# Optimization experiments

Measured on AMD Instinct MI355X. Metric: run time of the kernel, lower is better.

## Reference

```python
import jax, jax.numpy as jnp
import numpy as np

N_NODES = 50000
N_EDGES = 1_600_000
C = 128
K = 10


def setup_inputs() -> dict:
    key = jax.random.key(0)
    k1, k2, k3, k4 = jax.random.split(key, 4)
    x = jax.random.normal(k1, (N_NODES, C), dtype=jnp.float32)
    coeffs = jax.random.normal(k2, (K + 1,), dtype=jnp.float32) * 0.3
    src = jax.random.randint(k3, (N_EDGES,), 0, N_NODES, dtype=jnp.int64)
    dst = jax.random.randint(k4, (N_EDGES,), 0, N_NODES, dtype=jnp.int64)
    edge_index = jnp.stack([src, dst], axis=0)
    return {"x": x, "coeffs": coeffs, "edge_index": edge_index}


def _gcn_norm(edge_index, num_nodes, dtype):
    """Add self-loops, return (src, dst, norm) with norm = d^-1/2[src]*d^-1/2[dst]."""
    loop = jnp.arange(num_nodes, dtype=edge_index.dtype)
    src = jnp.concatenate([edge_index[0], loop])
    dst = jnp.concatenate([edge_index[1], loop])
    ones = jnp.ones(src.shape[0], dtype=dtype)
    deg = jax.ops.segment_sum(ones, dst, num_segments=num_nodes)
    dinv = jnp.where(deg > 0, jax.lax.rsqrt(deg), 0.0).astype(dtype)
    norm = dinv[src] * dinv[dst]  # [E+N]
    return src, dst, norm


def reference(x, coeffs, edge_index):
    """GPR/Arnoldi polynomial propagation:
       hidden = sum_{k=0..K} coeffs[k] * A_hat^k x, A_hat = D^-1/2 (A+I) D^-1/2."""
    n = x.shape[0]
    src, dst, norm = _gcn_norm(edge_index, n, x.dtype)

    def step(carry, gamma):
        xc, hid = carry
        msg = xc[src] * norm[:, None]                       # gather + scale
        xn = jax.ops.segment_sum(msg, dst, num_segments=n)  # scatter-add
        return (xn, hid + gamma * xn), None

    hidden0 = coeffs[0] * x
    (_, hidden), _ = jax.lax.scan(step, (x, hidden0), coeffs[1:])
    return hidden
```

## Files before the change

### kernel.cpp

```cpp
#include <hip/hip_runtime.h>
#include <hip/hip_fp16.h>

#define C 128
#define HC 64
#define NBUCK 256
#define NSLICE 8
#define NCHUNK 512
#define BCH 64
#define MAXNPS 8192

typedef float f4_t __attribute__((ext_vector_type(4)));

__global__ __launch_bounds__(256)
void pcount_kernel(const int* __restrict__ dst, int* __restrict__ pcnt, int E, int nps) {
    int chunk = blockIdx.x;
    const int per = (E + NCHUNK - 1) / NCHUNK;
    int beg = chunk * per;
    int end = beg + per; if (end > E) end = E;
    __shared__ int lc[NSLICE];
    if (threadIdx.x < NSLICE) lc[threadIdx.x] = 0;
    __syncthreads();
    for (int e = beg + threadIdx.x; e < end; e += 256) {
        int s = dst[e] / nps;
        atomicAdd(&lc[s], 1);
    }
    __syncthreads();
    if (threadIdx.x < NSLICE) pcnt[chunk * NSLICE + threadIdx.x] = lc[threadIdx.x];
}

__global__ __launch_bounds__(256)
void pscan_kernel(const int* __restrict__ pcnt, int* __restrict__ poffs,
                  int* __restrict__ sbase, int E) {
    __shared__ int part[256];
    int t = threadIdx.x;
    int vals[16];
    int sum = 0;
    #pragma unroll
    for (int i = 0; i < 16; ++i) {
        int key = t * 16 + i;
        int s = key >> 9;
        int c = key & (NCHUNK - 1);
        vals[i] = pcnt[c * NSLICE + s];
        sum += vals[i];
    }
    part[t] = sum;
    __syncthreads();
    for (int off = 1; off < 256; off <<= 1) {
        int v = 0;
        if (t >= off) v = part[t - off];
        __syncthreads();
        if (t >= off) part[t] += v;
        __syncthreads();
    }
    int run = (t == 0) ? 0 : part[t - 1];
    #pragma unroll
    for (int i = 0; i < 16; ++i) {
        poffs[t * 16 + i] = run;
        run += vals[i];
    }
    __syncthreads();
    if (t < NSLICE) sbase[t] = poffs[t << 9];
    if (t == NSLICE) sbase[NSLICE] = E;
}

__global__ __launch_bounds__(256)
void ppart_kernel(const int* __restrict__ src, const int* __restrict__ dst,
                  const int* __restrict__ poffs, unsigned int* __restrict__ pedges,
                  int E, int nps) {
    int chunk = blockIdx.x;
    const int per = (E + NCHUNK - 1) / NCHUNK;
    int beg = chunk * per;
    int end = beg + per; if (end > E) end = E;
    __shared__ int lcur[NSLICE];
    if (threadIdx.x < NSLICE) lcur[threadIdx.x] = poffs[threadIdx.x * NCHUNK + chunk];
    __syncthreads();
    for (int e = beg + threadIdx.x; e < end; e += 256) {
        int d = dst[e];
        int s = d / nps;
        int pos = atomicAdd(&lcur[s], 1);
        pedges[pos] = ((unsigned)(d - s * nps) << 16) | (unsigned)src[e];
    }
}

__global__ __launch_bounds__(256)
void bcount_kernel(const unsigned int* __restrict__ pedges, const int* __restrict__ sbase,
                   int* __restrict__ phist, int N, int nps) {
    int s = blockIdx.x & 7;
    int c = blockIdx.x >> 3;
    int lo = sbase[s], hi = sbase[s + 1];
    int len = hi - lo;
    int per = (len + BCH - 1) / BCH;
    int beg = lo + c * per;
    int end = beg + per; if (end > hi) end = hi;
    __shared__ int h[MAXNPS];
    int base_node = s * nps;
    int nn = nps; if (base_node + nn > N) nn = N - base_node;
    for (int i = threadIdx.x; i < nn; i += 256) h[i] = 0;
    __syncthreads();
    for (int e = beg + threadIdx.x; e < end; e += 256) {
        unsigned int u = pedges[e];
        atomicAdd(&h[u >> 16], 1);
    }
    __syncthreads();
    int* out = phist + (size_t)c * N + base_node;
    for (int i = threadIdx.x; i < nn; i += 256) out[i] = h[i];
}

__global__ void merge1_kernel(const int* __restrict__ phist, int* __restrict__ cnt, int N) {
    int i = blockIdx.x * blockDim.x + threadIdx.x;
    if (i >= N) return;
    int s = 0;
    #pragma unroll 8
    for (int c = 0; c < BCH; ++c) s += phist[(size_t)c * N + i];
    cnt[i] = s;
}

__global__ void merge2_kernel(const int* __restrict__ phist, const int* __restrict__ offsets,
                              int* __restrict__ pbase, int N) {
    int i = blockIdx.x * blockDim.x + threadIdx.x;
    if (i >= N) return;
    int run = offsets[i];
    #pragma unroll 8
    for (int c = 0; c < BCH; ++c) {
        pbase[(size_t)c * N + i] = run;
        run += phist[(size_t)c * N + i];
    }
}

__global__ __launch_bounds__(256)
void pscatter_kernel(const unsigned int* __restrict__ pedges, const int* __restrict__ sbase,
                     const int* __restrict__ pbase, unsigned short* __restrict__ srcs16,
                     int N, int nps) {
    int s = blockIdx.x & 7;
    int c = blockIdx.x >> 3;
    int lo = sbase[s], hi = sbase[s + 1];
    int len = hi - lo;
    int per = (len + BCH - 1) / BCH;
    int beg = lo + c * per;
    int end = beg + per; if (end > hi) end = hi;
    __shared__ int lcur[MAXNPS];
    int base_node = s * nps;
    int nn = nps; if (base_node + nn > N) nn = N - base_node;
    const int* pb = pbase + (size_t)c * N + base_node;
    for (int i = threadIdx.x; i < nn; i += 256) lcur[i] = pb[i];
    __syncthreads();
    for (int e = beg + threadIdx.x; e < end; e += 256) {
        unsigned int u = pedges[e];
        int pos = atomicAdd(&lcur[u >> 16], 1);
        srcs16[pos] = (unsigned short)(u & 0xffffu);
    }
}

__global__ void scan_reduce_kernel(const int* __restrict__ cnt, int* __restrict__ psum, int n) {
    __shared__ int s[256];
    int t = threadIdx.x;
    int i = blockIdx.x * 256 + t;
    s[t] = (i < n) ? cnt[i] : 0;
    __syncthreads();
    for (int off = 128; off > 0; off >>= 1) {
        if (t < off) s[t] += s[t + off];
        __syncthreads();
    }
    if (t == 0) psum[blockIdx.x] = s[0];
}

__global__ void scan_partials_kernel(const int* __restrict__ psum, int* __restrict__ bpre,
                                     int* __restrict__ offsets, int n, int nb) {
    __shared__ int s[256];
    int t = threadIdx.x;
    s[t] = (t < nb) ? psum[t] : 0;
    __syncthreads();
    for (int off = 1; off < 256; off <<= 1) {
        int v = 0;
        if (t >= off) v = s[t - off];
        __syncthreads();
        if (t >= off) s[t] += v;
        __syncthreads();
    }
    bpre[t] = (t == 0) ? 0 : s[t - 1];
    if (t == 255) offsets[n] = s[255];
}

__global__ void scan_apply_kernel(const int* __restrict__ cnt, const int* __restrict__ bpre,
                                  int* __restrict__ offsets, int* __restrict__ cursor,
                                  float* __restrict__ dinv, int n) {
    __shared__ int s[256];
    int t = threadIdx.x;
    int i = blockIdx.x * 256 + t;
    int c = (i < n) ? cnt[i] : 0;
    s[t] = c;
    __syncthreads();
    for (int off = 1; off < 256; off <<= 1) {
        int v = 0;
        if (t >= off) v = s[t - off];
        __syncthreads();
        if (t >= off) s[t] += v;
        __syncthreads();
    }
    if (i < n) {
        int excl = bpre[blockIdx.x] + s[t] - c;
        offsets[i] = excl;
        cursor[i]  = excl;
        dinv[i]    = rsqrtf((float)(c + 1));
    }
}

__global__ void hist_zero_kernel(int* __restrict__ hist) { hist[threadIdx.x] = 0; }

__global__ void hist_kernel(const int* __restrict__ cnt, int* __restrict__ hist, int n) {
    __shared__ int lh[NBUCK];
    int t = threadIdx.x;
    lh[t] = 0;
    __syncthreads();
    for (int i = blockIdx.x * blockDim.x + t; i < n; i += gridDim.x * blockDim.x) {
        int d = cnt[i]; if (d > NBUCK - 1) d = NBUCK - 1;
        atomicAdd(&lh[d], 1);
    }
    __syncthreads();
    int c = lh[t];
    if (c) atomicAdd(&hist[t], c);
}

__global__ void hist_scan_kernel(const int* __restrict__ hist, int* __restrict__ bcur) {
    __shared__ int s[256];
    int t = threadIdx.x;
    s[t] = hist[t];
    __syncthreads();
    for (int off = 1; off < 256; off <<= 1) {
        int v = 0;
        if (t >= off) v = s[t - off];
        __syncthreads();
        if (t >= off) s[t] += v;
        __syncthreads();
    }
    bcur[t] = (t == 0) ? 0 : s[t - 1];
}

__global__ void perm_kernel(const int* __restrict__ cnt, int* __restrict__ bcur,
                            int* __restrict__ perm, int n) {
    __shared__ int lhist[NBUCK];
    __shared__ int lbase[NBUCK];
    int t = threadIdx.x;
    lhist[t] = 0;
    __syncthreads();
    int i = blockIdx.x * 256 + t;
    int d = 0, lr = 0;
    if (i < n) {
        d = cnt[i]; if (d > NBUCK - 1) d = NBUCK - 1;
        lr = atomicAdd(&lhist[d], 1);
    }
    __syncthreads();
    int c = lhist[t];
    if (c > 0) lbase[t] = atomicAdd(&bcur[t], c);
    __syncthreads();
    if (i < n) perm[lbase[d] + lr] = i;
}

__global__ void zero_cnt_kernel(int* __restrict__ cnt, int n) {
    int i = blockIdx.x * blockDim.x + threadIdx.x;
    if (i < n) cnt[i] = 0;
}

__global__ void count_kernel(const int* __restrict__ dst, int* __restrict__ cnt,
                             int E, int nps) {
    int slice = blockIdx.x & 7;
    int chunk = blockIdx.x >> 3;
    int nchunks = gridDim.x >> 3;
    int per = (E + nchunks - 1) / nchunks;
    int beg = chunk * per;
    int end = beg + per; if (end > E) end = E;
    int lo = slice * nps, hi = lo + nps;
    for (int e = beg + threadIdx.x; e < end; e += blockDim.x) {
        int d = dst[e];
        if (d >= lo && d < hi) atomicAdd(&cnt[d], 1);
    }
}

__global__ void scatter_kernel(const int* __restrict__ src, const int* __restrict__ dst,
                               int* __restrict__ cursor, int* __restrict__ sorted_src,
                               int E, int nps) {
    int slice = blockIdx.x & 7;
    int chunk = blockIdx.x >> 3;
    int nchunks = gridDim.x >> 3;
    int per = (E + nchunks - 1) / nchunks;
    int beg = chunk * per;
    int end = beg + per; if (end > E) end = E;
    int lo = slice * nps, hi = lo + nps;
    for (int e = beg + threadIdx.x; e < end; e += blockDim.x) {
        int d = dst[e];
        if (d >= lo && d < hi) {
            int pos = atomicAdd(&cursor[d], 1);
            sorted_src[pos] = src[e];
        }
    }
}

__global__ void init_kernel(const float* __restrict__ x, const float* __restrict__ coeffs,
                            const float* __restrict__ dinv, float* __restrict__ hidden,
                            unsigned short* __restrict__ ya, unsigned short* __restrict__ yb,
                            int N) {
    int i = blockIdx.x * blockDim.x + threadIdx.x;
    if (i >= N * 16) return;
    int node = i >> 4;
    int g = i & 15;
    float dv = dinv[node];
    const float4* xp = (const float4*)(x + (size_t)node * C + g * 8);
    float4 x0 = xp[0], x1 = xp[1];
    if (hidden) {
        float g0 = coeffs[0];
        float4* hp = (float4*)(hidden + (size_t)node * C + g * 8);
        hp[0] = make_float4(g0 * x0.x, g0 * x0.y, g0 * x0.z, g0 * x0.w);
        hp[1] = make_float4(g0 * x1.x, g0 * x1.y, g0 * x1.z, g0 * x1.w);
    }
    __half2 p0 = __floats2half2_rn(dv * x0.x, dv * x0.y);
    __half2 p1 = __floats2half2_rn(dv * x0.z, dv * x0.w);
    __half2 p2 = __floats2half2_rn(dv * x1.x, dv * x1.y);
    __half2 p3 = __floats2half2_rn(dv * x1.z, dv * x1.w);
    uint4 u;
    u.x = *reinterpret_cast<unsigned int*>(&p0);
    u.y = *reinterpret_cast<unsigned int*>(&p1);
    u.z = *reinterpret_cast<unsigned int*>(&p2);
    u.w = *reinterpret_cast<unsigned int*>(&p3);
    unsigned short* yp = (g < 8) ? ya : yb;
    int jj = g & 7;
    ((uint4*)yp)[(size_t)node * 8 + jj] = u;
}

__device__ __forceinline__ void acc8(float* a, uint4 u) {
    __half2* h = (__half2*)&u;
    #pragma unroll
    for (int i = 0; i < 4; ++i) {
        float2 f = __half22float2(h[i]);
        a[2 * i]     += f.x;
        a[2 * i + 1] += f.y;
    }
}

template<typename IdxT>
__global__ __launch_bounds__(256)
void prop2_kernel(const unsigned short* __restrict__ yin0, const unsigned short* __restrict__ yin1,
                  unsigned short* __restrict__ yout0, unsigned short* __restrict__ yout1,
                  float* __restrict__ hidden, const float* __restrict__ coeffs, int k,
                  const int* __restrict__ offsets, const IdxT* __restrict__ srcs,
                  const float* __restrict__ dinv, const int* __restrict__ perm, int n) {
    int bid  = blockIdx.x;
    int xcd  = bid & 7;
    int half = xcd >> 2;
    int q    = (bid >> 3) * 4 + (xcd & 3);
    int t = threadIdx.x;
    int lane = t & 63;
    int grp  = lane >> 3;
    int j    = lane & 7;
    int slot = q * 32 + (t >> 6) * 8 + grp;
    if (slot >= n) return;
    int v = perm[slot];
    int beg = offsets[v];
    int end = offsets[v + 1];
    float dv = dinv[v];
    float gamma = coeffs[k];

    const uint4* base = (const uint4*)(half ? yin1 : yin0);
    float A0[8] = {0,0,0,0,0,0,0,0};
    float A1[8] = {0,0,0,0,0,0,0,0};
    float A2[8] = {0,0,0,0,0,0,0,0};
    float A3[8] = {0,0,0,0,0,0,0,0};

    int e = beg;
    for (; e + 8 <= end; e += 8) {
        int s0 = (int)srcs[e],     s1 = (int)srcs[e + 1];
        int s2 = (int)srcs[e + 2], s3 = (int)srcs[e + 3];
        int s4 = (int)srcs[e + 4], s5 = (int)srcs[e + 5];
        int s6 = (int)srcs[e + 6], s7 = (int)srcs[e + 7];
        uint4 u0 = base[(size_t)s0 * 8 + j];
        uint4 u1 = base[(size_t)s1 * 8 + j];
        uint4 u2 = base[(size_t)s2 * 8 + j];
        uint4 u3 = base[(size_t)s3 * 8 + j];
        uint4 u4 = base[(size_t)s4 * 8 + j];
        uint4 u5 = base[(size_t)s5 * 8 + j];
        uint4 u6 = base[(size_t)s6 * 8 + j];
        uint4 u7 = base[(size_t)s7 * 8 + j];
        acc8(A0, u0); acc8(A1, u1); acc8(A2, u2); acc8(A3, u3);
        acc8(A0, u4); acc8(A1, u5); acc8(A2, u6); acc8(A3, u7);
    }
    for (; e + 4 <= end; e += 4) {
        int s0 = (int)srcs[e],     s1 = (int)srcs[e + 1];
        int s2 = (int)srcs[e + 2], s3 = (int)srcs[e + 3];
        uint4 u0 = base[(size_t)s0 * 8 + j];
        uint4 u1 = base[(size_t)s1 * 8 + j];
        uint4 u2 = base[(size_t)s2 * 8 + j];
        uint4 u3 = base[(size_t)s3 * 8 + j];
        acc8(A0, u0); acc8(A1, u1); acc8(A2, u2); acc8(A3, u3);
    }
    for (; e < end; ++e) {
        uint4 u = base[(size_t)srcs[e] * 8 + j];
        acc8(A0, u);
    }
    uint4 us = base[(size_t)v * 8 + j];
    acc8(A1, us);

    float xn[8];
    #pragma unroll
    for (int i = 0; i < 8; ++i)
        xn[i] = dv * ((A0[i] + A1[i]) + (A2[i] + A3[i]));

    if (hidden) {
        f4_t* hp = (f4_t*)(hidden + (size_t)v * C + half * HC + j * 8);
        f4_t h0 = __builtin_nontemporal_load(hp);
        f4_t h1 = __builtin_nontemporal_load(hp + 1);
        h0.x += gamma * xn[0]; h0.y += gamma * xn[1]; h0.z += gamma * xn[2]; h0.w += gamma * xn[3];
        h1.x += gamma * xn[4]; h1.y += gamma * xn[5]; h1.z += gamma * xn[6]; h1.w += gamma * xn[7];
        __builtin_nontemporal_store(h0, hp);
        __builtin_nontemporal_store(h1, hp + 1);
    }

    __half2 p0 = __floats2half2_rn(dv * xn[0], dv * xn[1]);
    __half2 p1 = __floats2half2_rn(dv * xn[2], dv * xn[3]);
    __half2 p2 = __floats2half2_rn(dv * xn[4], dv * xn[5]);
    __half2 p3 = __floats2half2_rn(dv * xn[6], dv * xn[7]);
    uint4 u;
    u.x = *reinterpret_cast<unsigned int*>(&p0);
    u.y = *reinterpret_cast<unsigned int*>(&p1);
    u.z = *reinterpret_cast<unsigned int*>(&p2);
    u.w = *reinterpret_cast<unsigned int*>(&p3);
    unsigned short* yout = half ? yout1 : yout0;
    ((uint4*)yout)[(size_t)v * 8 + j] = u;
}

__global__ void final_kernel(const float* __restrict__ x, const float* __restrict__ coeffs,
                             const float* __restrict__ dinv, const unsigned short* __restrict__ ybig,
                             float* __restrict__ hidden, int N, int K) {
    int i = blockIdx.x * blockDim.x + threadIdx.x;
    if (i >= N * 16) return;
    int node = i >> 4;
    int g = i & 15;
    int half = g >> 3;
    int jj = g & 7;
    float g0 = coeffs[0];
    float rdv = 1.0f / dinv[node];
    const float4* xp = (const float4*)(x + (size_t)node * C + g * 8);
    float4 x0 = xp[0], x1 = xp[1];
    float a[8] = {g0 * x0.x, g0 * x0.y, g0 * x0.z, g0 * x0.w,
                  g0 * x1.x, g0 * x1.y, g0 * x1.z, g0 * x1.w};
    const uint4* yb = (const uint4*)ybig;
    size_t bstride = (size_t)N * 8;
    size_t row = (size_t)node * 8 + jj;
    for (int k = 1; k <= K; ++k) {
        float s = coeffs[k] * rdv;
        uint4 u = yb[(size_t)(2 * k + half) * bstride + row];
        __half2* h = (__half2*)&u;
        #pragma unroll
        for (int q2 = 0; q2 < 4; ++q2) {
            float2 f = __half22float2(h[q2]);
            a[2 * q2]     += s * f.x;
            a[2 * q2 + 1] += s * f.y;
        }
    }
    float4* hp = (float4*)(hidden + (size_t)node * C + g * 8);
    hp[0] = make_float4(a[0], a[1], a[2], a[3]);
    hp[1] = make_float4(a[4], a[5], a[6], a[7]);
}

extern "C" void kernel_launch(void* const* d_in, const int* in_sizes, int n_in,
                              void* d_out, int out_size, void* d_ws, size_t ws_size,
                              hipStream_t stream) {
    const float* x      = (const float*)d_in[0];
    const float* coeffs = (const float*)d_in[1];
    const int*   edge   = (const int*)d_in[2];

    const int N = in_sizes[0] / C;
    const int K = in_sizes[1] - 1;
    const int E = in_sizes[2] / 2;
    const int* src = edge;
    const int* dst = edge + E;

    char* ws = (char*)d_ws;
    auto alloc = [&](size_t bytes) -> void* {
        void* p = (void*)ws;
        ws += (bytes + 255) & ~(size_t)255;
        return p;
    };
    int*   cnt        = (int*)alloc((size_t)N * 4);
    int*   offsets    = (int*)alloc((size_t)(N + 1) * 4);
    int*   cursor     = (int*)alloc((size_t)N * 4);
    int*   sorted_src = (int*)alloc((size_t)E * 4);
    float* dinv       = (float*)alloc((size_t)N * 4);
    int*   psum       = (int*)alloc(256 * 4);
    int*   bpre       = (int*)alloc(256 * 4);
    int*   hist       = (int*)alloc(NBUCK * 4);
    int*   bcur       = (int*)alloc(NBUCK * 4);
    int*   perm       = (int*)alloc((size_t)N * 4);
    unsigned short* srcs16 = (unsigned short*)alloc((size_t)E * 2);
    unsigned int*   pedges = (unsigned int*)alloc((size_t)E * 4);
    int*   pcnt   = (int*)alloc((size_t)NCHUNK * NSLICE * 4);
    int*   poffs  = (int*)alloc((size_t)NCHUNK * NSLICE * 4);
    int*   sbase  = (int*)alloc((NSLICE + 1) * 4);
    int*   phist  = (int*)alloc((size_t)BCH * N * 4);
    int*   pbase  = (int*)alloc((size_t)BCH * N * 4);

    const size_t NBelems  = (size_t)N * HC;
    const size_t bufbytes = NBelems * 2;
    size_t misc_used = (size_t)(ws - (char*)d_ws);
    const int nbuf_deferred = 2 * (K + 1);
    bool deferred = (ws_size >= misc_used + (size_t)nbuf_deferred * bufbytes + 4096);
    unsigned short* ybig = (unsigned short*)alloc((size_t)(deferred ? nbuf_deferred : 4) * bufbytes);
    auto ybuf = [&](int p, int h) -> unsigned short* {
        return ybig + ((size_t)(2 * p + h)) * NBelems;
    };

    const int B = 256;
    const int nb = (N + 255) / 256;
    const int nps = (N + NSLICE - 1) / NSLICE;
    const bool fastpre = (N <= 65536) && (nps <= MAXNPS);

    if (fastpre) {
        pcount_kernel<<<NCHUNK, B, 0, stream>>>(dst, pcnt, E, nps);
        pscan_kernel<<<1, B, 0, stream>>>(pcnt, poffs, sbase, E);
        ppart_kernel<<<NCHUNK, B, 0, stream>>>(src, dst, poffs, pedges, E, nps);
        bcount_kernel<<<8 * BCH, B, 0, stream>>>(pedges, sbase, phist, N, nps);
        merge1_kernel<<<nb, B, 0, stream>>>(phist, cnt, N);
        scan_reduce_kernel<<<nb, 256, 0, stream>>>(cnt, psum, N);
        scan_partials_kernel<<<1, 256, 0, stream>>>(psum, bpre, offsets, N, nb);
        scan_apply_kernel<<<nb, 256, 0, stream>>>(cnt, bpre, offsets, cursor, dinv, N);
        merge2_kernel<<<nb, B, 0, stream>>>(phist, offsets, pbase, N);
        hist_zero_kernel<<<1, NBUCK, 0, stream>>>(hist);
        hist_kernel<<<64, 256, 0, stream>>>(cnt, hist, N);
        hist_scan_kernel<<<1, NBUCK, 0, stream>>>(hist, bcur);
        perm_kernel<<<nb, 256, 0, stream>>>(cnt, bcur, perm, N);
        pscatter_kernel<<<8 * BCH, B, 0, stream>>>(pedges, sbase, pbase, srcs16, N, nps);
    } else {
        const int slice_grid = 8 * 256;
        zero_cnt_kernel<<<(N + B - 1) / B, B, 0, stream>>>(cnt, N);
        count_kernel<<<slice_grid, B, 0, stream>>>(dst, cnt, E, nps);
        scan_reduce_kernel<<<nb, 256, 0, stream>>>(cnt, psum, N);
        scan_partials_kernel<<<1, 256, 0, stream>>>(psum, bpre, offsets, N, nb);
        scan_apply_kernel<<<nb, 256, 0, stream>>>(cnt, bpre, offsets, cursor, dinv, N);
        hist_zero_kernel<<<1, NBUCK, 0, stream>>>(hist);
        hist_kernel<<<64, 256, 0, stream>>>(cnt, hist, N);
        hist_scan_kernel<<<1, NBUCK, 0, stream>>>(hist, bcur);
        perm_kernel<<<nb, 256, 0, stream>>>(cnt, bcur, perm, N);
        scatter_kernel<<<slice_grid, B, 0, stream>>>(src, dst, cursor, sorted_src, E, nps);
    }

    float* hidden = (float*)d_out;
    float* hid_for_prop = deferred ? nullptr : hidden;
    init_kernel<<<((size_t)N * 16 + B - 1) / B, B, 0, stream>>>(
        x, coeffs, dinv, hid_for_prop, ybuf(0, 0), ybuf(0, 1), N);

    const int pgrid = (N + 31) / 32;
    const int grid2 = 8 * ((pgrid + 3) / 4);
    for (int k = 1; k <= K; ++k) {
        int pin  = deferred ? (k - 1) : ((k - 1) & 1);
        int pout = deferred ? k       : (k & 1);
        if (fastpre) {
            prop2_kernel<unsigned short><<<grid2, B, 0, stream>>>(
                ybuf(pin, 0), ybuf(pin, 1), ybuf(pout, 0), ybuf(pout, 1),
                hid_for_prop, coeffs, k, offsets, srcs16, dinv, perm, N);
        } else {
            prop2_kernel<int><<<grid2, B, 0, stream>>>(
                ybuf(pin, 0), ybuf(pin, 1), ybuf(pout, 0), ybuf(pout, 1),
                hid_for_prop, coeffs, k, offsets, sorted_src, dinv, perm, N);
        }
    }

    if (deferred) {
        final_kernel<<<((size_t)N * 16 + B - 1) / B, B, 0, stream>>>(
            x, coeffs, dinv, ybig, hidden, N, K);
    }
}
```

Before: 588.2 us.

## Pre-partition edges by source slice before destination partitioning; reverse degree-bucket order

Adds a first partition pass that groups edges by source-node slice into a packed dst<<16|src buffer. The existing destination partition then runs over this buffer, so within each destination slice the sources come out roughly ordered by slice. The aim is better gather locality on the x rows during propagation. It also changes the degree-bucket scan to give descending offsets, so high-degree nodes are scheduled first. This costs three extra preprocessing launches and one more E-sized buffer pass.

New measurement: 541.6 us. 7.9% less time.

```diff
diff --git a/kernel.cpp b/kernel.cpp
--- a/kernel.cpp
+++ b/kernel.cpp
@@ -11,8 +11,9 @@
 
 typedef float f4_t __attribute__((ext_vector_type(4)));
 
-__global__ __launch_bounds__(256)
-void pcount_kernel(const int* __restrict__ dst, int* __restrict__ pcnt, int E, int nps) {
+
+__global__ __launch_bounds__(256)
+void s0count_kernel(const int* __restrict__ src, int* __restrict__ s0cnt, int E, int snps) {
     int chunk = blockIdx.x;
     const int per = (E + NCHUNK - 1) / NCHUNK;
     int beg = chunk * per;
@@ -21,11 +22,30 @@
     if (threadIdx.x < NSLICE) lc[threadIdx.x] = 0;
     __syncthreads();
     for (int e = beg + threadIdx.x; e < end; e += 256) {
-        int s = dst[e] / nps;
+        int s = src[e] / snps;
         atomicAdd(&lc[s], 1);
     }
     __syncthreads();
-    if (threadIdx.x < NSLICE) pcnt[chunk * NSLICE + threadIdx.x] = lc[threadIdx.x];
+    if (threadIdx.x < NSLICE) s0cnt[chunk * NSLICE + threadIdx.x] = lc[threadIdx.x];
+}
+
+__global__ __launch_bounds__(256)
+void s0part_kernel(const int* __restrict__ src, const int* __restrict__ dst,
+                   const int* __restrict__ s0offs, unsigned int* __restrict__ edges0,
+                   int E, int snps) {
+    int chunk = blockIdx.x;
+    const int per = (E + NCHUNK - 1) / NCHUNK;
+    int beg = chunk * per;
+    int end = beg + per; if (end > E) end = E;
+    __shared__ int lcur[NSLICE];
+    if (threadIdx.x < NSLICE) lcur[threadIdx.x] = s0offs[threadIdx.x * NCHUNK + chunk];
+    __syncthreads();
+    for (int e = beg + threadIdx.x; e < end; e += 256) {
+        int sv = src[e];
+        int s = sv / snps;
+        int pos = atomicAdd(&lcur[s], 1);
+        edges0[pos] = ((unsigned)dst[e] << 16) | (unsigned)sv;
+    }
 }
 
 __global__ __launch_bounds__(256)
@@ -64,9 +84,26 @@
 }
 
 __global__ __launch_bounds__(256)
-void ppart_kernel(const int* __restrict__ src, const int* __restrict__ dst,
-                  const int* __restrict__ poffs, unsigned int* __restrict__ pedges,
-                  int E, int nps) {
+void pcount2_kernel(const unsigned int* __restrict__ edges0, int* __restrict__ pcnt,
+                    int E, int nps) {
+    int chunk = blockIdx.x;
+    const int per = (E + NCHUNK - 1) / NCHUNK;
+    int beg = chunk * per;
+    int end = beg + per; if (end > E) end = E;
+    __shared__ int lc[NSLICE];
+    if (threadIdx.x < NSLICE) lc[threadIdx.x] = 0;
+    __syncthreads();
+    for (int e = beg + threadIdx.x; e < end; e += 256) {
+        int s = (int)(edges0[e] >> 16) / nps;
+        atomicAdd(&lc[s], 1);
+    }
+    __syncthreads();
+    if (threadIdx.x < NSLICE) pcnt[chunk * NSLICE + threadIdx.x] = lc[threadIdx.x];
+}
+
+__global__ __launch_bounds__(256)
+void ppart2_kernel(const unsigned int* __restrict__ edges0, const int* __restrict__ poffs,
+                   unsigned int* __restrict__ pedges, int E, int nps) {
     int chunk = blockIdx.x;
     const int per = (E + NCHUNK - 1) / NCHUNK;
     int beg = chunk * per;
@@ -75,10 +112,11 @@
     if (threadIdx.x < NSLICE) lcur[threadIdx.x] = poffs[threadIdx.x * NCHUNK + chunk];
     __syncthreads();
     for (int e = beg + threadIdx.x; e < end; e += 256) {
-        int d = dst[e];
+        unsigned int u = edges0[e];
+        int d = (int)(u >> 16);
         int s = d / nps;
         int pos = atomicAdd(&lcur[s], 1);
-        pedges[pos] = ((unsigned)(d - s * nps) << 16) | (unsigned)src[e];
+        pedges[pos] = ((unsigned)(d - s * nps) << 16) | (u & 0xffffu);
     }
 }
 
@@ -233,7 +271,8 @@
         if (t >= off) s[t] += v;
         __syncthreads();
     }
-    bcur[t] = (t == 0) ? 0 : s[t - 1];
+    int total = s[255];
+    bcur[t] = total - s[t];
 }
 
 __global__ void perm_kernel(const int* __restrict__ cnt, int* __restrict__ bcur,
@@ -491,9 +530,13 @@
     int*   perm       = (int*)alloc((size_t)N * 4);
     unsigned short* srcs16 = (unsigned short*)alloc((size_t)E * 2);
     unsigned int*   pedges = (unsigned int*)alloc((size_t)E * 4);
+    unsigned int*   edges0 = (unsigned int*)alloc((size_t)E * 4);
     int*   pcnt   = (int*)alloc((size_t)NCHUNK * NSLICE * 4);
     int*   poffs  = (int*)alloc((size_t)NCHUNK * NSLICE * 4);
     int*   sbase  = (int*)alloc((NSLICE + 1) * 4);
+    int*   s0cnt  = (int*)alloc((size_t)NCHUNK * NSLICE * 4);
+    int*   s0offs = (int*)alloc((size_t)NCHUNK * NSLICE * 4);
+    int*   s0base = (int*)alloc((NSLICE + 1) * 4);
     int*   phist  = (int*)alloc((size_t)BCH * N * 4);
     int*   pbase  = (int*)alloc((size_t)BCH * N * 4);
 
@@ -510,12 +553,16 @@
     const int B = 256;
     const int nb = (N + 255) / 256;
     const int nps = (N + NSLICE - 1) / NSLICE;
+    const int snps = nps;
     const bool fastpre = (N <= 65536) && (nps <= MAXNPS);
 
     if (fastpre) {
-        pcount_kernel<<<NCHUNK, B, 0, stream>>>(dst, pcnt, E, nps);
+        s0count_kernel<<<NCHUNK, B, 0, stream>>>(src, s0cnt, E, snps);
+        pscan_kernel<<<1, B, 0, stream>>>(s0cnt, s0offs, s0base, E);
+        s0part_kernel<<<NCHUNK, B, 0, stream>>>(src, dst, s0offs, edges0, E, snps);
+        pcount2_kernel<<<NCHUNK, B, 0, stream>>>(edges0, pcnt, E, nps);
         pscan_kernel<<<1, B, 0, stream>>>(pcnt, poffs, sbase, E);
-        ppart_kernel<<<NCHUNK, B, 0, stream>>>(src, dst, poffs, pedges, E, nps);
+        ppart2_kernel<<<NCHUNK, B, 0, stream>>>(edges0, poffs, pedges, E, nps);
         bcount_kernel<<<8 * BCH, B, 0, stream>>>(pedges, sbase, phist, N, nps);
         merge1_kernel<<<nb, B, 0, stream>>>(phist, cnt, N);
         scan_reduce_kernel<<<nb, 256, 0, stream>>>(cnt, psum, N);
```
